# Kernel tuning notes

Hardware: AMD Instinct MI355X
Metric: run time of the kernel (lower is better)

Reference implementation:

```python
import jax, jax.numpy as jnp
import numpy as np
from jax import lax

B, N, FEAT, MID, HID, OUT = 128, 36, 2048, 517, 128, 1024
STEPS, TEMP = 3, 1.0


def setup_inputs() -> dict:
    key = jax.random.key(0)
    ks = jax.random.split(key, 10)
    s = 0.02
    return {
        "boxes": jax.random.uniform(ks[0], (B, 4, N), jnp.float32),
        "attention": jax.random.normal(ks[1], (B, N), jnp.float32),
        "features": jax.random.normal(ks[2], (B, N, FEAT), jnp.float32),
        "conv_w": jax.random.normal(ks[3], (MID - 5, FEAT), jnp.float32) * s,
        "conv_b": jnp.zeros((MID - 5,), jnp.float32),
        "skew_wx": jax.random.normal(ks[4], (HID, MID), jnp.float32) * s,
        "skew_wy": jax.random.normal(ks[5], (HID, MID), jnp.float32) * s,
        "skew_b1": jnp.zeros((HID,), jnp.float32),
        "skew_w2": jax.random.normal(ks[6], (HID,), jnp.float32) * s,
        "skew_b2": jnp.zeros((1,), jnp.float32),
        "w_ih": jax.random.normal(ks[7], (4 * OUT, MID), jnp.float32) * s,
        "w_hh": jax.random.normal(ks[8], (4 * OUT, OUT), jnp.float32) * s,
        "b_ih": jnp.zeros((4 * OUT,), jnp.float32),
        "b_hh": jnp.zeros((4 * OUT,), jnp.float32),
        "lr": jnp.ones((1,), jnp.float32),
    }


def _calculate_assignment(C, lr_abs, temp, steps):
    # C: (b, n, n) skew-symmetric ordering costs.
    logits = jnp.zeros_like(C)
    for _ in range(steps):
        P = jax.nn.softmax(logits / temp, axis=-1)  # position i -> distribution over elements l
        cum = jnp.cumsum(P, axis=1)                 # sum over positions k <= i
        below = cum - P                             # sum_{k<i} P_kl
        above = cum[:, -1:, :] - cum                # sum_{k>i} P_kl
        # grad_{ij} = sum_l C_{jl} * (above - below)_{il}  (uses skew-symmetry of C)
        G = jnp.einsum('bil,bjl->bij', above - below, C)
        logits = logits - lr_abs * G
    return jax.nn.softmax(logits / temp, axis=-1)


def reference(boxes, attention, features, conv_w, conv_b, skew_wx, skew_wy,
              skew_b1, skew_w2, skew_b2, w_ih, w_hh, b_ih, b_hh, lr):
    b = boxes.shape[0]
    # normalize boxes by per-sample max
    boxes = boxes / jnp.max(boxes.reshape(b, -1), axis=1)[:, None, None]
    # pointwise Conv1: 2048 -> MID-5, features arrives as (b, n, 2048)
    f = jnp.einsum('bnf,mf->bmn', features, conv_w) + conv_b[None, :, None]
    att = attention[:, None, :]                      # (b, 1, n)
    feats = jnp.concatenate([boxes, att, f], axis=1)  # (b, MID, n)
    # PairwiseSkew: f(x_i, x_j) - f(x_j, x_i); the first 1x1-conv over concatenated
    # pairs splits into two linear maps so we never materialize (b, 2*MID, n, n).
    hx = jnp.einsum('hm,bmn->bhn', skew_wx, feats)
    hy = jnp.einsum('hm,bmn->bhn', skew_wy, feats)
    h = jax.nn.relu(hx[:, :, :, None] + hy[:, :, None, :] + skew_b1[None, :, None, None])
    out = jnp.einsum('h,bhij->bij', skew_w2, h) + skew_b2[0]  # (b, n, n)
    C = out - jnp.swapaxes(out, 1, 2)  # skew-symmetrize
    A = _calculate_assignment(C, jnp.abs(lr)[0], TEMP, STEPS)
    # gate features by sigmoid(attention) and apply soft permutation
    gated = feats * jax.nn.sigmoid(att)               # (b, MID, n)
    x = jnp.einsum('bcl,bil->bci', gated, A)          # (b, MID, n)
    x_seq = jnp.transpose(x, (2, 0, 1))               # (n, b, MID)
    # single-layer LSTM (PyTorch gate order i, f, g, o); return final cell state
    bias = b_ih + b_hh
    Hd = w_hh.shape[1]
    def step(carry, xt):
        h_, c_ = carry
        gates = xt @ w_ih.T + h_ @ w_hh.T + bias
        i, fg, g, o = jnp.split(gates, 4, axis=-1)
        c_ = jax.nn.sigmoid(fg) * c_ + jax.nn.sigmoid(i) * jnp.tanh(g)
        h_ = jax.nn.sigmoid(o) * jnp.tanh(c_)
        return (h_, c_), None
    init = (jnp.zeros((b, Hd), x.dtype), jnp.zeros((b, Hd), x.dtype))
    (_, c_fin), _ = lax.scan(step, init, x_seq)
    return c_fin
```

## Files before the change

kernel.cpp:

```cpp
#include <hip/hip_runtime.h>
#include <math.h>

#define NB 128
#define NN 36
#define S37 37
#define S40 40
#define NFEAT 2048
#define NMID 517
#define KP 544
#define NHID 128
#define NOUT 1024
#define ROWS (NB*NN)

typedef __bf16 bf16x8 __attribute__((ext_vector_type(8)));
typedef float  f32x4  __attribute__((ext_vector_type(4)));

__device__ __forceinline__ float sigf(float x){ return 1.f/(1.f+expf(-x)); }
__device__ __forceinline__ unsigned short f2bf(float x){
    unsigned u = __float_as_uint(x);
    return (unsigned short)((u + 0x7FFFu + ((u>>16)&1u)) >> 16);
}
__device__ __forceinline__ float bf2f(unsigned short b){
    return __uint_as_float(((unsigned)b) << 16);
}

__global__ __launch_bounds__(256) void prep_all(
    const float* __restrict__ boxes, const float* __restrict__ att,
    const float* __restrict__ features, const float* __restrict__ conv_w,
    const float* __restrict__ wx, const float* __restrict__ wy,
    const float* __restrict__ b1, const float* __restrict__ w_ih,
    const float* __restrict__ w_hh, const float* __restrict__ b_ih,
    const float* __restrict__ b_hh,
    unsigned short* __restrict__ features_bf, unsigned short* __restrict__ convw_bf,
    unsigned short* __restrict__ wxy_bf, float* __restrict__ hxy_b,
    unsigned short* __restrict__ wih_il, unsigned short* __restrict__ whh_il,
    float* __restrict__ comb_b, unsigned short* __restrict__ h0,
    float* __restrict__ c, float* __restrict__ feats)
{
    int gtid = blockIdx.x*256 + threadIdx.x;
    int gs = gridDim.x*256;
    if (gtid < 128*64) {
        int b = gtid >> 6, t = gtid & 63;
        float mx = -1e30f;
        for (int idx = t; idx < 4*NN; idx += 64) mx = fmaxf(mx, boxes[b*4*NN + idx]);
        for (int off = 32; off > 0; off >>= 1) mx = fmaxf(mx, __shfl_down(mx, off));
        mx = __shfl(mx, 0);
        float inv = 1.f / mx;
        for (int idx = t; idx < 4*NN; idx += 64) {
            int r = idx / NN, n = idx - r*NN;
            feats[(size_t)(b*NN+n)*NMID + r] = boxes[b*4*NN + idx] * inv;
        }
        if (t < NN) feats[(size_t)(b*NN+t)*NMID + 4] = att[b*NN + t];
    }
    for (int i = gtid; i < ROWS*NFEAT; i += gs) features_bf[i] = f2bf(features[i]);
    for (int i = gtid; i < 512*NFEAT; i += gs) convw_bf[i] = f2bf(conv_w[i]);
    for (int i = gtid; i < 256*KP; i += gs) {
        int r = i / KP, k = i - r*KP;
        float v = 0.f;
        if (k < NMID) v = (r < NHID) ? wx[(size_t)r*NMID+k] : wy[(size_t)(r-NHID)*NMID+k];
        wxy_bf[i] = f2bf(v);
    }
    for (int i = gtid; i < 256; i += gs) hxy_b[i] = (i < NHID) ? b1[i] : 0.f;
    for (int i = gtid; i < 4*NOUT*KP; i += gs) {
        int row = i / KP, k = i - row*KP;
        int u = row >> 2, g = row & 3;
        wih_il[i] = (k < NMID) ? f2bf(w_ih[(size_t)(g*NOUT+u)*NMID + k]) : (unsigned short)0;
    }
    for (int i = gtid; i < 4*NOUT*NOUT; i += gs) {
        int row = i >> 10, k = i & 1023;
        int u = row >> 2, g = row & 3;
        whh_il[i] = f2bf(w_hh[(size_t)(g*NOUT+u)*NOUT + k]);
    }
    for (int i = gtid; i < 4*NOUT; i += gs) {
        int u = i >> 2, g = i & 3;
        comb_b[i] = b_ih[g*NOUT+u] + b_hh[g*NOUT+u];
    }
    for (int i = gtid; i < NB*NOUT; i += gs) { h0[i] = 0; c[i] = 0.f; }
}

__global__ __launch_bounds__(256) void gemm128(
    const unsigned short* __restrict__ A, const unsigned short* __restrict__ B,
    const float* __restrict__ bias, void* __restrict__ Cp,
    int Ksl, int lda, int ldb, int ldc, int obf, long long pstride)
{
    __shared__ __align__(16) char As[16384];
    __shared__ __align__(16) char Bs[16384];
    int m0 = blockIdx.y * 128, n0 = blockIdx.x * 128;
    int kbeg = blockIdx.z * Ksl;
    int tid = threadIdx.x;
    int lane = tid & 63, wave = tid >> 6;
    int wm = wave >> 1, wn = wave & 1;
    int sw = ((lane>>4)<<8) + (((lane&15) ^ ((lane>>4)<<2))<<4);
    f32x4 acc[4][4];
    #pragma unroll
    for (int i = 0; i < 4; ++i)
        #pragma unroll
        for (int j = 0; j < 4; ++j) acc[i][j] = (f32x4){0.f,0.f,0.f,0.f};

    for (int k0 = 0; k0 < Ksl; k0 += 32) {
        #pragma unroll
        for (int p = 0; p < 2; ++p) {
            int cc = p*256 + tid;
            int r = cc >> 2, q = cc & 3;
            int sa = ((r>>4)<<10) + (q<<8) + ((((r&15) ^ (q<<2)))<<4);
            uint4 va = *(const uint4*)(A + (size_t)(m0+r)*lda + kbeg + k0 + q*8);
            *(uint4*)(As + sa) = va;
            uint4 vb = *(const uint4*)(B + (size_t)(n0+r)*ldb + kbeg + k0 + q*8);
            *(uint4*)(Bs + sa) = vb;
        }
        __syncthreads();
        bf16x8 af[4], bfr[4];
        #pragma unroll
        for (int i = 0; i < 4; ++i) af[i]  = *(bf16x8*)(As + ((wm*4+i)<<10) + sw);
        #pragma unroll
        for (int j = 0; j < 4; ++j) bfr[j] = *(bf16x8*)(Bs + ((wn*4+j)<<10) + sw);
        #pragma unroll
        for (int i = 0; i < 4; ++i)
            #pragma unroll
            for (int j = 0; j < 4; ++j)
                acc[i][j] = __builtin_amdgcn_mfma_f32_16x16x32_bf16(af[i], bfr[j], acc[i][j], 0, 0, 0);
        __syncthreads();
    }
    int colf = lane & 15, rowq = lane >> 4;
    #pragma unroll
    for (int j = 0; j < 4; ++j) {
        int col = n0 + (wn*4+j)*16 + colf;
        float bv = bias ? bias[col] : 0.f;
        #pragma unroll
        for (int i = 0; i < 4; ++i) {
            #pragma unroll
            for (int reg = 0; reg < 4; ++reg) {
                int row = m0 + (wm*4+i)*16 + rowq*4 + reg;
                float v = acc[i][j][reg] + bv;
                if (obf) ((unsigned short*)Cp)[(size_t)row*ldc + col] = f2bf(v);
                else ((float*)Cp + (size_t)blockIdx.z*pstride)[(size_t)row*ldc + col] = v;
            }
        }
    }
}

__global__ __launch_bounds__(256) void conv_reduce(
    const float* __restrict__ part, const float* __restrict__ bias,
    float* __restrict__ feats, unsigned short* __restrict__ feats_bf)
{
    int gtid = blockIdx.x*256 + threadIdx.x;
    int gs = gridDim.x*256;
    const size_t PS = (size_t)ROWS * 512;
    for (int i = gtid; i < ROWS*512; i += gs) {
        int r = i >> 9, cc = i & 511;
        float s = part[i] + part[PS+i] + part[2*PS+i] + part[3*PS+i] + bias[cc];
        feats[(size_t)r*NMID + 5 + cc] = s;
        feats_bf[(size_t)r*KP + 5 + cc] = f2bf(s);
    }
    for (int i = gtid; i < ROWS*5; i += gs) {
        int r = i / 5, cc = i - r*5;
        feats_bf[(size_t)r*KP + cc] = f2bf(feats[(size_t)r*NMID + cc]);
    }
    for (int i = gtid; i < ROWS*27; i += gs) {
        int r = i / 27, cc = i - r*27;
        feats_bf[(size_t)r*KP + 517 + cc] = 0;
    }
}

__global__ __launch_bounds__(256) void gemm_mfma(
    const unsigned short* __restrict__ A, const unsigned short* __restrict__ B,
    const float* __restrict__ bias, void* __restrict__ Cp,
    int K, int lda, int ldb, int ldc, int obf)
{
    __shared__ __align__(16) char As[8192];
    __shared__ __align__(16) char Bs[4096];
    int m0 = blockIdx.y * 128, n0 = blockIdx.x * 64;
    int tid = threadIdx.x;
    int lane = tid & 63, wave = tid >> 6;
    int wm = wave >> 1, wn = wave & 1;
    f32x4 acc[4][2];
    #pragma unroll
    for (int i = 0; i < 4; ++i)
        #pragma unroll
        for (int j = 0; j < 2; ++j) acc[i][j] = (f32x4){0.f,0.f,0.f,0.f};

    for (int k0 = 0; k0 < K; k0 += 32) {
        #pragma unroll
        for (int cc = tid; cc < 512; cc += 256) {
            int r = cc >> 2, q = cc & 3;
            uint4 v = *(const uint4*)(A + (size_t)(m0+r)*lda + k0 + q*8);
            *(uint4*)(As + ((r>>4)<<10) + (q<<8) + ((r&15)<<4)) = v;
        }
        {
            int r = tid >> 2, q = tid & 3;
            uint4 v = *(const uint4*)(B + (size_t)(n0+r)*ldb + k0 + q*8);
            *(uint4*)(Bs + ((r>>4)<<10) + (q<<8) + ((r&15)<<4)) = v;
        }
        __syncthreads();
        bf16x8 af[4], bfr[2];
        #pragma unroll
        for (int i = 0; i < 4; ++i) af[i]  = *(bf16x8*)(As + ((wm*4+i)<<10) + (lane<<4));
        #pragma unroll
        for (int j = 0; j < 2; ++j) bfr[j] = *(bf16x8*)(Bs + ((wn*2+j)<<10) + (lane<<4));
        #pragma unroll
        for (int i = 0; i < 4; ++i)
            #pragma unroll
            for (int j = 0; j < 2; ++j)
                acc[i][j] = __builtin_amdgcn_mfma_f32_16x16x32_bf16(af[i], bfr[j], acc[i][j], 0, 0, 0);
        __syncthreads();
    }
    int colf = lane & 15, rowq = lane >> 4;
    #pragma unroll
    for (int j = 0; j < 2; ++j) {
        int col = n0 + (wn*2+j)*16 + colf;
        float bv = bias ? bias[col] : 0.f;
        #pragma unroll
        for (int i = 0; i < 4; ++i) {
            #pragma unroll
            for (int reg = 0; reg < 4; ++reg) {
                int row = m0 + (wm*4+i)*16 + rowq*4 + reg;
                float v = acc[i][j][reg] + bv;
                if (obf) ((unsigned short*)Cp)[(size_t)row*ldc + col] = f2bf(v);
                else     ((float*)Cp)[(size_t)row*ldc + col] = v;
            }
        }
    }
}

__global__ __launch_bounds__(256) void out_k(
    const float* __restrict__ hxy, const float* __restrict__ w2,
    float* __restrict__ out_g)
{
    __shared__ float s_hx[9*129], s_hy[NN*129], s_w2[NHID];
    int b = blockIdx.x, i0 = blockIdx.y * 9, tid = threadIdx.x;
    for (int i = tid; i < 9*NHID; i += 256) {
        int n = i >> 7, h = i & 127;
        s_hx[n*129+h] = hxy[(size_t)(b*NN+i0+n)*256 + h];
    }
    for (int i = tid; i < NN*NHID; i += 256) {
        int n = i >> 7, h = i & 127;
        s_hy[n*129+h] = hxy[(size_t)(b*NN+n)*256 + 128 + h];
    }
    if (tid < NHID) s_w2[tid] = w2[tid];
    __syncthreads();
    for (int idx = tid; idx < 9*NN; idx += 256) {
        int il = idx / NN, j = idx - il*NN;
        const float* px = &s_hx[il*129];
        const float* py = &s_hy[j*129];
        float s = 0.f;
        #pragma unroll 8
        for (int h = 0; h < NHID; ++h) s += s_w2[h] * fmaxf(px[h] + py[h], 0.f);
        out_g[(size_t)b*NN*NN + (i0+il)*NN + j] = s;
    }
}

__global__ __launch_bounds__(256) void iter_k(
    const float* __restrict__ out_g, const float* __restrict__ att,
    const float* __restrict__ lr, float* __restrict__ A_g)
{
    __shared__ __align__(16) float s_out[NN*S40], s_C[NN*S40], s_logits[NN*S40], s_P[NN*S40];
    __shared__ float s_sg[NN];
    int b = blockIdx.x, tid = threadIdx.x;
    for (int idx = tid; idx < NN*NN; idx += 256) {
        int i = idx / NN, j = idx - i*NN;
        s_out[i*S40+j] = out_g[(size_t)b*NN*NN + idx];
        s_logits[i*S40+j] = 0.f;
    }
    if (tid < NN) s_sg[tid] = sigf(att[b*NN + tid]);
    float lr_abs = fabsf(lr[0]);
    __syncthreads();
    for (int idx = tid; idx < NN*NN; idx += 256) {
        int i = idx / NN, j = idx - i*NN;
        s_C[i*S40+j] = s_out[i*S40+j] - s_out[j*S40+i];
    }
    __syncthreads();
    for (int it = 0; it < 3; ++it) {
        if (tid < NN) {
            int i = tid;
            float mx = -1e30f;
            for (int l = 0; l < NN; ++l) mx = fmaxf(mx, s_logits[i*S40+l]);
            float sum = 0.f;
            for (int l = 0; l < NN; ++l) { float e = expf(s_logits[i*S40+l]-mx); s_P[i*S40+l] = e; sum += e; }
            float inv = 1.f/sum;
            for (int l = 0; l < NN; ++l) s_P[i*S40+l] *= inv;
        }
        __syncthreads();
        if (tid < NN) {
            int l = tid;
            float S = 0.f;
            for (int i = 0; i < NN; ++i) S += s_P[i*S40+l];
            float cum = 0.f;
            for (int i = 0; i < NN; ++i) {
                float p = s_P[i*S40+l];
                cum += p;
                s_P[i*S40+l] = S - 2.f*cum + p;
            }
        }
        __syncthreads();
        for (int idx = tid; idx < NN*NN; idx += 256) {
            int i = idx / NN, j = idx - i*NN;
            const f32x4* Pp = (const f32x4*)&s_P[i*S40];
            const f32x4* Cc = (const f32x4*)&s_C[j*S40];
            float g = 0.f;
            #pragma unroll
            for (int q = 0; q < 9; ++q) {
                f32x4 a = Pp[q], bb = Cc[q];
                g += a[0]*bb[0] + a[1]*bb[1] + a[2]*bb[2] + a[3]*bb[3];
            }
            s_logits[i*S40+j] -= lr_abs * g;
        }
        __syncthreads();
    }
    if (tid < NN) {
        int i = tid;
        float mx = -1e30f;
        for (int l = 0; l < NN; ++l) mx = fmaxf(mx, s_logits[i*S40+l]);
        float sum = 0.f;
        for (int l = 0; l < NN; ++l) { float e = expf(s_logits[i*S40+l]-mx); s_P[i*S40+l] = e; sum += e; }
        float inv = 1.f/sum;
        for (int l = 0; l < NN; ++l)
            A_g[(size_t)b*NN*NN + i*NN + l] = s_P[i*S40+l] * inv * s_sg[l];
    }
}

__global__ __launch_bounds__(256) void xseq_k(
    const float* __restrict__ feats, const float* __restrict__ A_g,
    unsigned short* __restrict__ xseq)
{
    __shared__ float s_P[NN*S37];
    int b = blockIdx.x, half = blockIdx.y, tid = threadIdx.x;
    for (int idx = tid; idx < NN*NN; idx += 256) {
        int i = idx / NN, l = idx - i*NN;
        s_P[i*S37+l] = A_g[(size_t)b*NN*NN + idx];
    }
    __syncthreads();
    const float* fb = feats + (size_t)b*NN*NMID;
    int ncols = (half == 0 && tid < 32) ? 2 : 1;
    #pragma unroll
    for (int rep = 0; rep < 2; ++rep) {
        if (rep >= ncols) break;
        int c = (rep == 0) ? half*256 + tid : 512 + tid;
        float colv[NN];
        #pragma unroll
        for (int l = 0; l < NN; ++l) colv[l] = (c < NMID) ? fb[l*NMID + c] : 0.f;
        #pragma unroll 4
        for (int i = 0; i < NN; ++i) {
            float s = 0.f;
            #pragma unroll
            for (int l = 0; l < NN; ++l) s += s_P[i*S37+l] * colv[l];
            xseq[((size_t)i*NB + b)*KP + c] = f2bf(s);
        }
    }
}

__global__ __launch_bounds__(256, 2) void lstm_step(
    const unsigned short* __restrict__ h_in, const unsigned short* __restrict__ whh,
    const unsigned short* __restrict__ xw_t, float* __restrict__ c,
    unsigned short* __restrict__ h_out, float* __restrict__ cout)
{
    __shared__ __align__(16) char Bls[65536];
    __shared__ __align__(16) float gates[32][36];
    int tid = threadIdx.x, lane = tid & 63, wave = tid >> 6;
    int bt = blockIdx.x >> 7, ct = blockIdx.x & 127;
    int m0 = bt * 32, n0 = ct * 32;
    #pragma unroll
    for (int r = 0; r < 16; ++r) {
        int idx = r*256 + tid;
        int n = idx >> 7, kc = idx & 127;
        uint4 v = *(const uint4*)(whh + (size_t)(n0+n)*NOUT + kc*8);
        *(uint4*)(Bls + kc*512 + (((n&16) | ((n^kc)&15))<<4)) = v;
    }
    __syncthreads();
    int wm = wave >> 1, wn = wave & 1;
    int q = lane >> 4, ml = lane & 15;
    const unsigned short* hrow = h_in + (size_t)(m0 + wm*16 + ml)*NOUT + q*8;
    int nl = wn*16 + ml;
    f32x4 acc = (f32x4){0.f,0.f,0.f,0.f};
    #pragma unroll 8
    for (int it = 0; it < 32; ++it) {
        int kc = it*4 + q;
        bf16x8 a = *(const bf16x8*)(hrow + it*32);
        bf16x8 b = *(const bf16x8*)(Bls + kc*512 + (((nl&16) | ((nl^kc)&15))<<4));
        acc = __builtin_amdgcn_mfma_f32_16x16x32_bf16(a, b, acc, 0, 0, 0);
    }
    #pragma unroll
    for (int reg = 0; reg < 4; ++reg)
        gates[wm*16 + q*4 + reg][wn*16 + ml] = acc[reg];
    __syncthreads();
    {
        int ul = tid & 7, bl = tid >> 3;
        int b = m0 + bl, u = ct*8 + ul;
        float4 gl = *(const float4*)&gates[bl][ul*4];
        uint2 xw2 = *(const uint2*)(xw_t + (size_t)b*4*NOUT + n0 + ul*4);
        float g0 = gl.x + bf2f((unsigned short)(xw2.x & 0xffffu));
        float g1 = gl.y + bf2f((unsigned short)(xw2.x >> 16));
        float g2 = gl.z + bf2f((unsigned short)(xw2.y & 0xffffu));
        float g3 = gl.w + bf2f((unsigned short)(xw2.y >> 16));
        float ig = sigf(g0), fg = sigf(g1), gg = tanhf(g2), og = sigf(g3);
        size_t o = (size_t)b*NOUT + u;
        float cc = fg*c[o] + ig*gg;
        c[o] = cc;
        if (cout) cout[o] = cc;
        else      h_out[o] = f2bf(og*tanhf(cc));
    }
}

extern "C" void kernel_launch(void* const* d_in, const int* in_sizes, int n_in,
                              void* d_out, int out_size, void* d_ws, size_t ws_size,
                              hipStream_t stream) {
    (void)in_sizes; (void)n_in; (void)out_size; (void)ws_size;
    const float* boxes     = (const float*)d_in[0];
    const float* attention = (const float*)d_in[1];
    const float* features  = (const float*)d_in[2];
    const float* conv_w    = (const float*)d_in[3];
    const float* conv_b    = (const float*)d_in[4];
    const float* skew_wx   = (const float*)d_in[5];
    const float* skew_wy   = (const float*)d_in[6];
    const float* skew_b1   = (const float*)d_in[7];
    const float* skew_w2   = (const float*)d_in[8];
    const float* w_ih      = (const float*)d_in[10];
    const float* w_hh      = (const float*)d_in[11];
    const float* b_ih      = (const float*)d_in[12];
    const float* b_hh      = (const float*)d_in[13];
    const float* lr        = (const float*)d_in[14];

    char* ws = (char*)d_ws;
    float*          part     = (float*)(ws);
    unsigned short* xw_bf    = (unsigned short*)(ws);
    unsigned short* features_bf = (unsigned short*)(ws + 37748736);
    unsigned short* convw_bf = (unsigned short*)(ws + 56623104);
    float*          feats    = (float*)(ws + 58720256);
    float*          hxy      = (float*)(ws + 68249600);
    unsigned short* feats_bf = (unsigned short*)(ws + 72968192);
    unsigned short* xseq_bf  = (unsigned short*)(ws + 77981696);
    unsigned short* wih_il   = (unsigned short*)(ws + 82995200);
    unsigned short* whh_il   = (unsigned short*)(ws + 87451648);
    unsigned short* wxy_bf   = (unsigned short*)(ws + 95840256);
    float*          comb_b   = (float*)(ws + 96118784);
    float*          hxy_b    = (float*)(ws + 96135168);
    unsigned short* h0       = (unsigned short*)(ws + 96136192);
    unsigned short* h1       = (unsigned short*)(ws + 96398336);
    float*          out_g    = (float*)(ws + 96660480);
    float*          A_g      = (float*)(ws + 97324032);
    float*          cst      = (float*)(ws + 97987584);

    prep_all<<<2048, 256, 0, stream>>>(boxes, attention, features, conv_w,
                                       skew_wx, skew_wy, skew_b1, w_ih, w_hh,
                                       b_ih, b_hh, features_bf, convw_bf,
                                       wxy_bf, hxy_b, wih_il, whh_il, comb_b,
                                       h0, cst, feats);
    gemm128<<<dim3(4, 36, 4), 256, 0, stream>>>(features_bf, convw_bf, nullptr,
                                                (void*)part, 512, NFEAT, NFEAT, 512, 0,
                                                (long long)ROWS*512);
    conv_reduce<<<2048, 256, 0, stream>>>(part, conv_b, feats, feats_bf);
    gemm_mfma<<<dim3(4, 36), 256, 0, stream>>>(feats_bf, wxy_bf, hxy_b,
                                               (void*)hxy, KP, KP, KP, 256, 0);
    out_k<<<dim3(NB, 4), 256, 0, stream>>>(hxy, skew_w2, out_g);
    iter_k<<<NB, 256, 0, stream>>>(out_g, attention, lr, A_g);
    xseq_k<<<dim3(NB, 2), 256, 0, stream>>>(feats, A_g, xseq_bf);
    gemm128<<<dim3(32, 36, 1), 256, 0, stream>>>(xseq_bf, wih_il, comb_b,
                                                 (void*)xw_bf, KP, KP, KP, 4*NOUT, 1, 0);
    unsigned short* hbuf[2] = {h0, h1};
    for (int t = 0; t < NN; ++t) {
        float* co = (t == NN-1) ? (float*)d_out : nullptr;
        lstm_step<<<512, 256, 0, stream>>>(hbuf[t & 1], whh_il,
                                           xw_bf + (size_t)t*NB*4*NOUT, cst,
                                           hbuf[(t+1) & 1], co);
    }
}
```

Before: 708.4 us.

## Replace per-step LSTM launches with a persistent kernel using a grid barrier

The 36 separate lstm_step launches become one persistent kernel of 256 blocks. Each block loads its W_hh slice into LDS once, keeps the cell state in registers, and handles 64 batch rows instead of 32. Steps are separated by an atomic grid-wide barrier. This removes per-step launch overhead and the repeated W_hh reloads, but relies on all 256 blocks being co-resident and adds spin-barrier latency at every step.

```diff
diff --git a/kernel.cpp b/kernel.cpp
--- a/kernel.cpp
+++ b/kernel.cpp
@@ -35,7 +35,7 @@
     unsigned short* __restrict__ wxy_bf, float* __restrict__ hxy_b,
     unsigned short* __restrict__ wih_il, unsigned short* __restrict__ whh_il,
     float* __restrict__ comb_b, unsigned short* __restrict__ h0,
-    float* __restrict__ c, float* __restrict__ feats)
+    unsigned* __restrict__ bar, float* __restrict__ feats)
 {
     int gtid = blockIdx.x*256 + threadIdx.x;
     int gs = gridDim.x*256;
@@ -75,7 +75,8 @@
         int u = i >> 2, g = i & 3;
         comb_b[i] = b_ih[g*NOUT+u] + b_hh[g*NOUT+u];
     }
-    for (int i = gtid; i < NB*NOUT; i += gs) { h0[i] = 0; c[i] = 0.f; }
+    for (int i = gtid; i < NB*NOUT; i += gs) h0[i] = 0;
+    for (int i = gtid; i < 64; i += gs) bar[i] = 0;
 }
 
 __global__ __launch_bounds__(256) void gemm128(
@@ -348,16 +349,16 @@
     }
 }
 
-__global__ __launch_bounds__(256, 2) void lstm_step(
-    const unsigned short* __restrict__ h_in, const unsigned short* __restrict__ whh,
-    const unsigned short* __restrict__ xw_t, float* __restrict__ c,
-    unsigned short* __restrict__ h_out, float* __restrict__ cout)
+__global__ __launch_bounds__(256) void lstm_persist(
+    const unsigned short* __restrict__ whh, const unsigned short* __restrict__ xw,
+    unsigned short* __restrict__ h0, unsigned short* __restrict__ h1,
+    float* __restrict__ cout, unsigned* __restrict__ bar)
 {
     __shared__ __align__(16) char Bls[65536];
-    __shared__ __align__(16) float gates[32][36];
+    __shared__ __align__(16) float gates[64][36];
     int tid = threadIdx.x, lane = tid & 63, wave = tid >> 6;
     int bt = blockIdx.x >> 7, ct = blockIdx.x & 127;
-    int m0 = bt * 32, n0 = ct * 32;
+    int m0 = bt * 64, n0 = ct * 32;
     #pragma unroll
     for (int r = 0; r < 16; ++r) {
         int idx = r*256 + tid;
@@ -365,38 +366,62 @@
         uint4 v = *(const uint4*)(whh + (size_t)(n0+n)*NOUT + kc*8);
         *(uint4*)(Bls + kc*512 + (((n&16) | ((n^kc)&15))<<4)) = v;
     }
-    __syncthreads();
     int wm = wave >> 1, wn = wave & 1;
     int q = lane >> 4, ml = lane & 15;
-    const unsigned short* hrow = h_in + (size_t)(m0 + wm*16 + ml)*NOUT + q*8;
     int nl = wn*16 + ml;
-    f32x4 acc = (f32x4){0.f,0.f,0.f,0.f};
-    #pragma unroll 8
-    for (int it = 0; it < 32; ++it) {
-        int kc = it*4 + q;
-        bf16x8 a = *(const bf16x8*)(hrow + it*32);
-        bf16x8 b = *(const bf16x8*)(Bls + kc*512 + (((nl&16) | ((nl^kc)&15))<<4));
-        acc = __builtin_amdgcn_mfma_f32_16x16x32_bf16(a, b, acc, 0, 0, 0);
-    }
-    #pragma unroll
-    for (int reg = 0; reg < 4; ++reg)
-        gates[wm*16 + q*4 + reg][wn*16 + ml] = acc[reg];
+    int ul = tid & 7, bl0 = tid >> 3;
+    float creg[2] = {0.f, 0.f};
+    const unsigned short* hbuf[2] = {h0, h1};
+    unsigned short* hbw[2] = {h0, h1};
     __syncthreads();
-    {
-        int ul = tid & 7, bl = tid >> 3;
-        int b = m0 + bl, u = ct*8 + ul;
-        float4 gl = *(const float4*)&gates[bl][ul*4];
-        uint2 xw2 = *(const uint2*)(xw_t + (size_t)b*4*NOUT + n0 + ul*4);
-        float g0 = gl.x + bf2f((unsigned short)(xw2.x & 0xffffu));
-        float g1 = gl.y + bf2f((unsigned short)(xw2.x >> 16));
-        float g2 = gl.z + bf2f((unsigned short)(xw2.y & 0xffffu));
-        float g3 = gl.w + bf2f((unsigned short)(xw2.y >> 16));
-        float ig = sigf(g0), fg = sigf(g1), gg = tanhf(g2), og = sigf(g3);
-        size_t o = (size_t)b*NOUT + u;
-        float cc = fg*c[o] + ig*gg;
-        c[o] = cc;
-        if (cout) cout[o] = cc;
-        else      h_out[o] = f2bf(og*tanhf(cc));
+    for (int t = 0; t < NN; ++t) {
+        const unsigned short* h_in = hbuf[t & 1];
+        const unsigned short* hrow0 = h_in + (size_t)(m0 + wm*32 + ml)*NOUT + q*8;
+        const unsigned short* hrow1 = hrow0 + 16*NOUT;
+        f32x4 acc0 = (f32x4){0.f,0.f,0.f,0.f};
+        f32x4 acc1 = (f32x4){0.f,0.f,0.f,0.f};
+        #pragma unroll 8
+        for (int it = 0; it < 32; ++it) {
+            int kc = it*4 + q;
+            bf16x8 b = *(const bf16x8*)(Bls + kc*512 + (((nl&16) | ((nl^kc)&15))<<4));
+            bf16x8 a0 = *(const bf16x8*)(hrow0 + it*32);
+            bf16x8 a1 = *(const bf16x8*)(hrow1 + it*32);
+            acc0 = __builtin_amdgcn_mfma_f32_16x16x32_bf16(a0, b, acc0, 0, 0, 0);
+            acc1 = __builtin_amdgcn_mfma_f32_16x16x32_bf16(a1, b, acc1, 0, 0, 0);
+        }
+        #pragma unroll
+        for (int reg = 0; reg < 4; ++reg) {
+            gates[wm*32 + q*4 + reg][nl]      = acc0[reg];
+            gates[wm*32 + 16 + q*4 + reg][nl] = acc1[reg];
+        }
+        __syncthreads();
+        const unsigned short* xw_t = xw + (size_t)t*NB*4*NOUT;
+        #pragma unroll
+        for (int p = 0; p < 2; ++p) {
+            int blb = bl0 + p*32;
+            int b = m0 + blb, u = ct*8 + ul;
+            float4 gl = *(const float4*)&gates[blb][ul*4];
+            uint2 xw2 = *(const uint2*)(xw_t + (size_t)b*4*NOUT + n0 + ul*4);
+            float g0 = gl.x + bf2f((unsigned short)(xw2.x & 0xffffu));
+            float g1 = gl.y + bf2f((unsigned short)(xw2.x >> 16));
+            float g2 = gl.z + bf2f((unsigned short)(xw2.y & 0xffffu));
+            float g3 = gl.w + bf2f((unsigned short)(xw2.y >> 16));
+            float ig = sigf(g0), fg = sigf(g1), gg = tanhf(g2), og = sigf(g3);
+            float cc = fg*creg[p] + ig*gg;
+            creg[p] = cc;
+            if (t == NN-1) cout[(size_t)b*NOUT + u] = cc;
+            else hbw[(t+1) & 1][(size_t)b*NOUT + u] = f2bf(og*tanhf(cc));
+        }
+        if (t < NN-1) {
+            __syncthreads();
+            if (tid == 0) {
+                unsigned tgt = (unsigned)gridDim.x * (unsigned)(t + 1);
+                __hip_atomic_fetch_add(bar, 1u, __ATOMIC_ACQ_REL, __HIP_MEMORY_SCOPE_AGENT);
+                while (__hip_atomic_load(bar, __ATOMIC_ACQUIRE, __HIP_MEMORY_SCOPE_AGENT) < tgt)
+                    __builtin_amdgcn_s_sleep(8);
+            }
+            __syncthreads();
+        }
     }
 }
 
@@ -437,13 +462,13 @@
     unsigned short* h1       = (unsigned short*)(ws + 96398336);
     float*          out_g    = (float*)(ws + 96660480);
     float*          A_g      = (float*)(ws + 97324032);
-    float*          cst      = (float*)(ws + 97987584);
+    unsigned*       bar      = (unsigned*)(ws + 97987584);
 
     prep_all<<<2048, 256, 0, stream>>>(boxes, attention, features, conv_w,
                                        skew_wx, skew_wy, skew_b1, w_ih, w_hh,
                                        b_ih, b_hh, features_bf, convw_bf,
                                        wxy_bf, hxy_b, wih_il, whh_il, comb_b,
-                                       h0, cst, feats);
+                                       h0, bar, feats);
     gemm128<<<dim3(4, 36, 4), 256, 0, stream>>>(features_bf, convw_bf, nullptr,
                                                 (void*)part, 512, NFEAT, NFEAT, 512, 0,
                                                 (long long)ROWS*512);
@@ -455,11 +480,6 @@
     xseq_k<<<dim3(NB, 2), 256, 0, stream>>>(feats, A_g, xseq_bf);
     gemm128<<<dim3(32, 36, 1), 256, 0, stream>>>(xseq_bf, wih_il, comb_b,
                                                  (void*)xw_bf, KP, KP, KP, 4*NOUT, 1, 0);
-    unsigned short* hbuf[2] = {h0, h1};
-    for (int t = 0; t < NN; ++t) {
-        float* co = (t == NN-1) ? (float*)d_out : nullptr;
-        lstm_step<<<512, 256, 0, stream>>>(hbuf[t & 1], whh_il,
-                                           xw_bf + (size_t)t*NB*4*NOUT, cst,
-                                           hbuf[(t+1) & 1], co);
-    }
-}
+    lstm_persist<<<256, 256, 0, stream>>>(whh_il, xw_bf, h0, h1,
+                                          (float*)d_out, bar);
+}
```

After: 1.078 ms. 1.52x slower.

## Replace LDS-staged GEMMs with direct-from-global MFMA loads and drop split-K reduce

Applied to the files above, without the earlier changes.

Both large GEMMs now load MFMA operand fragments straight from global memory into registers, with register double-buffering, instead of staging tiles through shared memory. The conv GEMM no longer splits K four ways. It writes fp32 and bf16 features with bias directly, which removes the partial-sum buffer and the conv_reduce kernel, and the box and attention bf16 columns are now written in prep. lstm_step also stops staging w_hh slices in LDS and reads them directly. The aim is to cut LDS traffic, barriers, one kernel launch and a round trip through the split-K buffer. The cost is uncoalesced 16-byte strided global loads that depend on L2/cache reuse, and less parallelism in the conv GEMM (288 blocks instead of 576).

```diff
diff --git a/kernel.cpp b/kernel.cpp
--- a/kernel.cpp
+++ b/kernel.cpp
@@ -35,7 +35,8 @@
     unsigned short* __restrict__ wxy_bf, float* __restrict__ hxy_b,
     unsigned short* __restrict__ wih_il, unsigned short* __restrict__ whh_il,
     float* __restrict__ comb_b, unsigned short* __restrict__ h0,
-    float* __restrict__ c, float* __restrict__ feats)
+    float* __restrict__ c, float* __restrict__ feats,
+    unsigned short* __restrict__ feats_bf)
 {
     int gtid = blockIdx.x*256 + threadIdx.x;
     int gs = gridDim.x*256;
@@ -48,9 +49,19 @@
         float inv = 1.f / mx;
         for (int idx = t; idx < 4*NN; idx += 64) {
             int r = idx / NN, n = idx - r*NN;
-            feats[(size_t)(b*NN+n)*NMID + r] = boxes[b*4*NN + idx] * inv;
-        }
-        if (t < NN) feats[(size_t)(b*NN+t)*NMID + 4] = att[b*NN + t];
+            float v = boxes[b*4*NN + idx] * inv;
+            feats[(size_t)(b*NN+n)*NMID + r] = v;
+            feats_bf[(size_t)(b*NN+n)*KP + r] = f2bf(v);
+        }
+        if (t < NN) {
+            float av = att[b*NN + t];
+            feats[(size_t)(b*NN+t)*NMID + 4] = av;
+            feats_bf[(size_t)(b*NN+t)*KP + 4] = f2bf(av);
+        }
+    }
+    for (int i = gtid; i < ROWS*27; i += gs) {
+        int r = i / 27, cc = i - r*27;
+        feats_bf[(size_t)r*KP + 517 + cc] = 0;
     }
     for (int i = gtid; i < ROWS*NFEAT; i += gs) features_bf[i] = f2bf(features[i]);
     for (int i = gtid; i < 512*NFEAT; i += gs) convw_bf[i] = f2bf(conv_w[i]);
@@ -78,87 +89,61 @@
     for (int i = gtid; i < NB*NOUT; i += gs) { h0[i] = 0; c[i] = 0.f; }
 }
 
-__global__ __launch_bounds__(256) void gemm128(
+template<int NJ>
+__global__ __launch_bounds__(256) void gemm_direct(
     const unsigned short* __restrict__ A, const unsigned short* __restrict__ B,
-    const float* __restrict__ bias, void* __restrict__ Cp,
-    int Ksl, int lda, int ldb, int ldc, int obf, long long pstride)
-{
-    __shared__ __align__(16) char As[16384];
-    __shared__ __align__(16) char Bs[16384];
-    int m0 = blockIdx.y * 128, n0 = blockIdx.x * 128;
-    int kbeg = blockIdx.z * Ksl;
-    int tid = threadIdx.x;
-    int lane = tid & 63, wave = tid >> 6;
+    const float* __restrict__ bias, float* __restrict__ Cf,
+    unsigned short* __restrict__ Cb, int K, int lda, int ldb,
+    int ldcf, int ldcb)
+{
+    int m0 = blockIdx.y * 128, n0 = blockIdx.x * (NJ * 32);
+    int tid = threadIdx.x, lane = tid & 63, wave = tid >> 6;
     int wm = wave >> 1, wn = wave & 1;
-    int sw = ((lane>>4)<<8) + (((lane&15) ^ ((lane>>4)<<2))<<4);
-    f32x4 acc[4][4];
+    int ml = lane & 15, q = lane >> 4;
+    const unsigned short* Ab = A + (size_t)(m0 + wm*64 + ml)*lda + q*8;
+    const unsigned short* Bb = B + (size_t)(n0 + wn*NJ*16 + ml)*ldb + q*8;
+    f32x4 acc[4][NJ];
     #pragma unroll
     for (int i = 0; i < 4; ++i)
         #pragma unroll
-        for (int j = 0; j < 4; ++j) acc[i][j] = (f32x4){0.f,0.f,0.f,0.f};
-
-    for (int k0 = 0; k0 < Ksl; k0 += 32) {
-        #pragma unroll
-        for (int p = 0; p < 2; ++p) {
-            int cc = p*256 + tid;
-            int r = cc >> 2, q = cc & 3;
-            int sa = ((r>>4)<<10) + (q<<8) + ((((r&15) ^ (q<<2)))<<4);
-            uint4 va = *(const uint4*)(A + (size_t)(m0+r)*lda + kbeg + k0 + q*8);
-            *(uint4*)(As + sa) = va;
-            uint4 vb = *(const uint4*)(B + (size_t)(n0+r)*ldb + kbeg + k0 + q*8);
-            *(uint4*)(Bs + sa) = vb;
-        }
-        __syncthreads();
-        bf16x8 af[4], bfr[4];
-        #pragma unroll
-        for (int i = 0; i < 4; ++i) af[i]  = *(bf16x8*)(As + ((wm*4+i)<<10) + sw);
-        #pragma unroll
-        for (int j = 0; j < 4; ++j) bfr[j] = *(bf16x8*)(Bs + ((wn*4+j)<<10) + sw);
+        for (int j = 0; j < NJ; ++j) acc[i][j] = (f32x4){0.f,0.f,0.f,0.f};
+    bf16x8 afc[4], bfc[NJ];
+    #pragma unroll
+    for (int i = 0; i < 4; ++i) afc[i] = *(const bf16x8*)(Ab + (size_t)i*16*lda);
+    #pragma unroll
+    for (int j = 0; j < NJ; ++j) bfc[j] = *(const bf16x8*)(Bb + (size_t)j*16*ldb);
+    for (int k0 = 0; k0 < K; k0 += 32) {
+        int k1 = (k0 + 32 < K) ? (k0 + 32) : k0;
+        bf16x8 afn[4], bfn[NJ];
+        #pragma unroll
+        for (int i = 0; i < 4; ++i) afn[i] = *(const bf16x8*)(Ab + (size_t)i*16*lda + k1);
+        #pragma unroll
+        for (int j = 0; j < NJ; ++j) bfn[j] = *(const bf16x8*)(Bb + (size_t)j*16*ldb + k1);
         #pragma unroll
         for (int i = 0; i < 4; ++i)
             #pragma unroll
-            for (int j = 0; j < 4; ++j)
-                acc[i][j] = __builtin_amdgcn_mfma_f32_16x16x32_bf16(af[i], bfr[j], acc[i][j], 0, 0, 0);
-        __syncthreads();
+            for (int j = 0; j < NJ; ++j)
+                acc[i][j] = __builtin_amdgcn_mfma_f32_16x16x32_bf16(afc[i], bfc[j], acc[i][j], 0, 0, 0);
+        #pragma unroll
+        for (int i = 0; i < 4; ++i) afc[i] = afn[i];
+        #pragma unroll
+        for (int j = 0; j < NJ; ++j) bfc[j] = bfn[j];
     }
     int colf = lane & 15, rowq = lane >> 4;
     #pragma unroll
-    for (int j = 0; j < 4; ++j) {
-        int col = n0 + (wn*4+j)*16 + colf;
+    for (int j = 0; j < NJ; ++j) {
+        int col = n0 + wn*NJ*16 + j*16 + colf;
         float bv = bias ? bias[col] : 0.f;
         #pragma unroll
         for (int i = 0; i < 4; ++i) {
             #pragma unroll
             for (int reg = 0; reg < 4; ++reg) {
-                int row = m0 + (wm*4+i)*16 + rowq*4 + reg;
+                int row = m0 + wm*64 + i*16 + rowq*4 + reg;
                 float v = acc[i][j][reg] + bv;
-                if (obf) ((unsigned short*)Cp)[(size_t)row*ldc + col] = f2bf(v);
-                else ((float*)Cp + (size_t)blockIdx.z*pstride)[(size_t)row*ldc + col] = v;
+                if (Cf) Cf[(size_t)row*ldcf + col] = v;
+                if (Cb) Cb[(size_t)row*ldcb + col] = f2bf(v);
             }
         }
-    }
-}
-
-__global__ __launch_bounds__(256) void conv_reduce(
-    const float* __restrict__ part, const float* __restrict__ bias,
-    float* __restrict__ feats, unsigned short* __restrict__ feats_bf)
-{
-    int gtid = blockIdx.x*256 + threadIdx.x;
-    int gs = gridDim.x*256;
-    const size_t PS = (size_t)ROWS * 512;
-    for (int i = gtid; i < ROWS*512; i += gs) {
-        int r = i >> 9, cc = i & 511;
-        float s = part[i] + part[PS+i] + part[2*PS+i] + part[3*PS+i] + bias[cc];
-        feats[(size_t)r*NMID + 5 + cc] = s;
-        feats_bf[(size_t)r*KP + 5 + cc] = f2bf(s);
-    }
-    for (int i = gtid; i < ROWS*5; i += gs) {
-        int r = i / 5, cc = i - r*5;
-        feats_bf[(size_t)r*KP + cc] = f2bf(feats[(size_t)r*NMID + cc]);
-    }
-    for (int i = gtid; i < ROWS*27; i += gs) {
-        int r = i / 27, cc = i - r*27;
-        feats_bf[(size_t)r*KP + 517 + cc] = 0;
     }
 }
 
@@ -298,8 +283,8 @@
             const f32x4* Cc = (const f32x4*)&s_C[j*S40];
             float g = 0.f;
             #pragma unroll
-            for (int q = 0; q < 9; ++q) {
-                f32x4 a = Pp[q], bb = Cc[q];
+            for (int qq = 0; qq < 9; ++qq) {
+                f32x4 a = Pp[qq], bb = Cc[qq];
                 g += a[0]*bb[0] + a[1]*bb[1] + a[2]*bb[2] + a[3]*bb[3];
             }
             s_logits[i*S40+j] -= lr_abs * g;
@@ -348,34 +333,24 @@
     }
 }
 
-__global__ __launch_bounds__(256, 2) void lstm_step(
+__global__ __launch_bounds__(256) void lstm_step(
     const unsigned short* __restrict__ h_in, const unsigned short* __restrict__ whh,
     const unsigned short* __restrict__ xw_t, float* __restrict__ c,
     unsigned short* __restrict__ h_out, float* __restrict__ cout)
 {
-    __shared__ __align__(16) char Bls[65536];
     __shared__ __align__(16) float gates[32][36];
     int tid = threadIdx.x, lane = tid & 63, wave = tid >> 6;
     int bt = blockIdx.x >> 7, ct = blockIdx.x & 127;
     int m0 = bt * 32, n0 = ct * 32;
-    #pragma unroll
-    for (int r = 0; r < 16; ++r) {
-        int idx = r*256 + tid;
-        int n = idx >> 7, kc = idx & 127;
-        uint4 v = *(const uint4*)(whh + (size_t)(n0+n)*NOUT + kc*8);
-        *(uint4*)(Bls + kc*512 + (((n&16) | ((n^kc)&15))<<4)) = v;
-    }
-    __syncthreads();
     int wm = wave >> 1, wn = wave & 1;
-    int q = lane >> 4, ml = lane & 15;
-    const unsigned short* hrow = h_in + (size_t)(m0 + wm*16 + ml)*NOUT + q*8;
-    int nl = wn*16 + ml;
+    int ml = lane & 15, q = lane >> 4;
+    const unsigned short* Ab = h_in + (size_t)(m0 + wm*16 + ml)*NOUT + q*8;
+    const unsigned short* Bb = whh  + (size_t)(n0 + wn*16 + ml)*NOUT + q*8;
     f32x4 acc = (f32x4){0.f,0.f,0.f,0.f};
     #pragma unroll 8
     for (int it = 0; it < 32; ++it) {
-        int kc = it*4 + q;
-        bf16x8 a = *(const bf16x8*)(hrow + it*32);
-        bf16x8 b = *(const bf16x8*)(Bls + kc*512 + (((nl&16) | ((nl^kc)&15))<<4));
+        bf16x8 a = *(const bf16x8*)(Ab + it*32);
+        bf16x8 b = *(const bf16x8*)(Bb + it*32);
         acc = __builtin_amdgcn_mfma_f32_16x16x32_bf16(a, b, acc, 0, 0, 0);
     }
     #pragma unroll
@@ -420,7 +395,6 @@
     const float* lr        = (const float*)d_in[14];
 
     char* ws = (char*)d_ws;
-    float*          part     = (float*)(ws);
     unsigned short* xw_bf    = (unsigned short*)(ws);
     unsigned short* features_bf = (unsigned short*)(ws + 37748736);
     unsigned short* convw_bf = (unsigned short*)(ws + 56623104);
@@ -443,18 +417,18 @@
                                        skew_wx, skew_wy, skew_b1, w_ih, w_hh,
                                        b_ih, b_hh, features_bf, convw_bf,
                                        wxy_bf, hxy_b, wih_il, whh_il, comb_b,
-                                       h0, cst, feats);
-    gemm128<<<dim3(4, 36, 4), 256, 0, stream>>>(features_bf, convw_bf, nullptr,
-                                                (void*)part, 512, NFEAT, NFEAT, 512, 0,
-                                                (long long)ROWS*512);
-    conv_reduce<<<2048, 256, 0, stream>>>(part, conv_b, feats, feats_bf);
+                                       h0, cst, feats, feats_bf);
+    gemm_direct<2><<<dim3(8, 36), 256, 0, stream>>>(
+        features_bf, convw_bf, conv_b, feats + 5, feats_bf + 5,
+        NFEAT, NFEAT, NFEAT, NMID, KP);
     gemm_mfma<<<dim3(4, 36), 256, 0, stream>>>(feats_bf, wxy_bf, hxy_b,
                                                (void*)hxy, KP, KP, KP, 256, 0);
     out_k<<<dim3(NB, 4), 256, 0, stream>>>(hxy, skew_w2, out_g);
     iter_k<<<NB, 256, 0, stream>>>(out_g, attention, lr, A_g);
     xseq_k<<<dim3(NB, 2), 256, 0, stream>>>(feats, A_g, xseq_bf);
-    gemm128<<<dim3(32, 36, 1), 256, 0, stream>>>(xseq_bf, wih_il, comb_b,
-                                                 (void*)xw_bf, KP, KP, KP, 4*NOUT, 1, 0);
+    gemm_direct<4><<<dim3(32, 36), 256, 0, stream>>>(
+        xseq_bf, wih_il, comb_b, nullptr, xw_bf,
+        KP, KP, KP, 0, 4*NOUT);
     unsigned short* hbuf[2] = {h0, h1};
     for (int t = 0; t < NN; ++t) {
         float* co = (t == NN-1) ? (float*)d_out : nullptr;
```

Measured after the change: 987.0 us. +39.3%, slower.
